# Kernel tuning notes

Hardware: AMD Instinct MI355X
Metric: run time of the kernel (lower is better)

The kernel has to match this reference:

```python
import jax, jax.numpy as jnp
import numpy as np

B = 4096       # batch
N_IN = 784     # input neurons
BANKS = 64     # banks per layer
L = 16         # layers of banks (layer 0 = input banks)
FAN = 8        # fan-out per source bank into next layer
D = 10         # n_neurons_per_hidd_bank
N_CONN = (L - 1) * BANKS * FAN  # total bank connections (7680)


def setup_inputs() -> dict:
    key = jax.random.key(0)
    ks = jax.random.split(key, 7)
    x = jax.random.normal(ks[0], (B, N_IN), jnp.float32)
    # input2hidden: Linear(N_IN, D, bias=True) for each input bank -> weight [D, N_IN]
    Wi = jax.random.normal(ks[1], (BANKS, D, N_IN), jnp.float32) / np.sqrt(N_IN).astype(np.float32)
    bi = jax.random.normal(ks[2], (BANKS, D), jnp.float32) * 0.1
    # per-edge gate: Linear(D, 1, bias=True); bias shifted so gates are a mix of open/closed
    Wg = jax.random.normal(ks[3], (L - 1, BANKS, FAN, D), jnp.float32) / np.sqrt(D).astype(np.float32)
    bg = jax.random.normal(ks[4], (L - 1, BANKS, FAN), jnp.float32) * 0.3 + 0.2
    # per-edge data: Linear(D, D, bias=False) -> weight [out=D, in=D]
    Wd = jax.random.normal(ks[5], (L - 1, BANKS, FAN, D, D), jnp.float32) / np.sqrt(D).astype(np.float32)
    # hidden2output: Linear(D, 1, bias=False) per output bank
    Wo = jax.random.normal(ks[6], (BANKS, D), jnp.float32) / np.sqrt(D).astype(np.float32)
    return {"x": x, "Wi": Wi, "bi": bi, "Wg": Wg, "bg": bg, "Wd": Wd, "Wo": Wo}


def reference(x, Wi, bi, Wg, bg, Wd, Wo):
    # forward_softgate with defaults: no batch norm, dropout p=0 (identity),
    # gates enabled (b_no_gates=False), positive gate loss, no gate_status.
    batch = x.shape[0]
    # static scatter targets: source bank s feeds banks (s+k)%BANKS of next layer
    s = np.arange(BANKS)[:, None]
    k = np.arange(FAN)[None, :]
    tgt = jnp.asarray(((s + k) % BANKS).reshape(-1))  # [BANKS*FAN]

    # input banks (layer 0); the target loop applies ReLU to every bank, incl. input banks
    acts = jax.nn.relu(jnp.einsum('bi,koi->bko', x, Wi) + bi)  # [B, BANKS, D]

    def layer(acts, w):
        wg, bgl, wd = w
        # gate: hardtanh(Linear(acts), 0, 1) per edge -> [B, BANKS, FAN]
        gate = jnp.clip(jnp.einsum('bsd,skd->bsk', acts, wg) + bgl, 0.0, 1.0)
        # data: Linear(D, D, bias=False); torch y = x @ W.T with W[out, in]
        data = jnp.einsum('bsd,sked->bske', acts, wd)  # [B, BANKS, FAN, D]
        contrib = (gate[..., None] * data).reshape(batch, BANKS * FAN, D)
        acc = jnp.zeros_like(acts).at[:, tgt].add(contrib)  # scatter-add into target banks
        new_acts = jax.nn.relu(acc)
        gate_sum = gate.sum(axis=(1, 2))                   # per-sample gate activity
        n_open = (gate > 0.0).sum().astype(jnp.float32)    # open-gate count
        return new_acts, (gate_sum, n_open)

    acts, (gate_sums, n_opens) = jax.lax.scan(layer, acts, (Wg, bg, Wd))
    total_gate_act = (gate_sums.sum(axis=0) / N_CONN)[:, None]          # [B, 1]
    prob_open_gate = n_opens.sum() / (N_CONN * batch)                   # scalar
    # output banks = last layer banks, Linear(D,1,bias=False) each, then ReLU
    output = jax.nn.relu(jnp.einsum('bkd,kd->bk', acts, Wo))            # [B, BANKS]
    return output, total_gate_act, prob_open_gate
```

## Files before the change

kernel.cpp:

```cpp
#include <hip/hip_runtime.h>
#include <type_traits>

#define NIN 784
#define BANKS 64
#define NLAYER 15
#define FAN 8
#define DD 10
#define NBF 640
#define NSW 4
#define NSB 8

#define BM 128
#define BN 64
#define BK 16

__global__ __launch_bounds__(256)
void input_gemm(const float* __restrict__ x, const float* __restrict__ Wi,
                const float* __restrict__ bi, float* __restrict__ acts)
{
    __shared__ float As[BK][BM + 4];
    __shared__ float Bs[BK][BN + 4];
    const int tid = threadIdx.x;
    const int tx = tid & 15, ty = tid >> 4;
    const int m0 = blockIdx.x * BM;
    const int n0 = blockIdx.y * BN;

    float acc[8][4];
#pragma unroll
    for (int i = 0; i < 8; ++i)
#pragma unroll
        for (int j = 0; j < 4; ++j) acc[i][j] = 0.f;

    for (int kb = 0; kb < NIN / BK; ++kb) {
#pragma unroll
        for (int i = 0; i < 2; ++i) {
            int flat = tid + 256 * i;
            int m = flat >> 2, kq = flat & 3;
            float4 v = *(const float4*)(x + (m0 + m) * NIN + kb * BK + kq * 4);
            As[kq*4+0][m] = v.x; As[kq*4+1][m] = v.y;
            As[kq*4+2][m] = v.z; As[kq*4+3][m] = v.w;
        }
        {
            int n = tid >> 2, kq = tid & 3;
            float4 v = *(const float4*)(Wi + (n0 + n) * NIN + kb * BK + kq * 4);
            Bs[kq*4+0][n] = v.x; Bs[kq*4+1][n] = v.y;
            Bs[kq*4+2][n] = v.z; Bs[kq*4+3][n] = v.w;
        }
        __syncthreads();
#pragma unroll
        for (int k = 0; k < BK; ++k) {
            float4 a0 = *(const float4*)(&As[k][ty*8]);
            float4 a1 = *(const float4*)(&As[k][ty*8+4]);
            float4 bb = *(const float4*)(&Bs[k][tx*4]);
            float av[8] = {a0.x,a0.y,a0.z,a0.w,a1.x,a1.y,a1.z,a1.w};
            float bv[4] = {bb.x,bb.y,bb.z,bb.w};
#pragma unroll
            for (int i = 0; i < 8; ++i)
#pragma unroll
                for (int j = 0; j < 4; ++j)
                    acc[i][j] = fmaf(av[i], bv[j], acc[i][j]);
        }
        __syncthreads();
    }
    float4 bv = *(const float4*)(bi + n0 + tx*4);
#pragma unroll
    for (int i = 0; i < 8; ++i) {
        int row = m0 + ty*8 + i;
        float4 o;
        o.x = fmaxf(acc[i][0] + bv.x, 0.f);
        o.y = fmaxf(acc[i][1] + bv.y, 0.f);
        o.z = fmaxf(acc[i][2] + bv.z, 0.f);
        o.w = fmaxf(acc[i][3] + bv.w, 0.f);
        *(float4*)(acts + row * NBF + n0 + tx*4) = o;
    }
}

__device__ __forceinline__ float f4c_rt(const float4& v, int c) {
    return c == 0 ? v.x : (c == 1 ? v.y : (c == 2 ? v.z : v.w));
}

typedef const __attribute__((address_space(1))) void gas_void;
typedef __attribute__((address_space(3))) void las_void;

__device__ __forceinline__ void gll16(const void* g, void* l) {
    __builtin_amdgcn_global_load_lds((gas_void*)g, (las_void*)l, 16, 0, 0);
}

#define NCH (NLAYER*FAN*28*64)
#define NBI (NLAYER*2*64)

__global__ __launch_bounds__(256)
void transpose_weights(const float* __restrict__ Wg, const float* __restrict__ bg,
                       const float* __restrict__ Wd,
                       float4* __restrict__ chunk_t, float4* __restrict__ bias_t)
{
    int tid = blockIdx.x * 256 + threadIdx.x;
    if (tid < NCH) {
        int b = tid & 63;
        int rk = tid >> 6;
        int r = rk % 28;
        int lk = rk / 28;
        int k = lk & 7;
        int l = lk >> 3;
        float4 v;
        if (r < 25) {
            v = ((const float4*)Wd)[(((size_t)(l*64+b)*8 + k)*25) + r];
        } else {
            int q = r - 25;
            size_t base = ((size_t)(l*64+b)*8 + k)*10 + 4*q;
            float t[4];
#pragma unroll
            for (int c = 0; c < 4; ++c)
                t[c] = (4*q + c < 10) ? Wg[base + c] : 0.f;
            v = make_float4(t[0], t[1], t[2], t[3]);
        }
        chunk_t[tid] = v;
    } else if (tid < NCH + NBI) {
        int t2 = tid - NCH;
        int b = t2 & 63;
        int q = (t2 >> 6) & 1;
        int l = t2 >> 7;
        bias_t[t2] = ((const float4*)bg)[(size_t)(l*64+b)*2 + q];
    }
}

template<bool CT>
__global__ __launch_bounds__(256, 2)
void routenet_v5(const float* __restrict__ acts0,
                 const float* __restrict__ x, const float* __restrict__ Wi,
                 const float* __restrict__ bi,
                 const float* __restrict__ Wg, const float* __restrict__ bg,
                 const float* __restrict__ Wd, const float* __restrict__ Wo,
                 const float4* __restrict__ chunk_t, const float4* __restrict__ bias_t,
                 float* __restrict__ out, unsigned int* __restrict__ nopen_g)
{
    __shared__ float4 wdstage[2][28][64];
    __shared__ float4 biasbuf[2][2][64];
    __shared__ float  exch[2][NSW][5][64];

    const int tid  = threadIdx.x;
    const int lane = tid & 63;
    const int w    = tid >> 6;
    const int g    = w & 1;
    const int h    = w >> 1;
    const int b0   = blockIdx.x * NSB + g * NSW;

    float a[NSW][DD];

    if (acts0) {
#pragma unroll
        for (int s = 0; s < NSW; ++s) {
            const float2* p = (const float2*)(acts0 + (size_t)(b0 + s) * NBF + lane * DD);
#pragma unroll
            for (int d2 = 0; d2 < 5; ++d2) {
                float2 v = p[d2];
                a[s][d2*2]   = v.x;
                a[s][d2*2+1] = v.y;
            }
        }
    } else {
        for (int s = 0; s < NSW; ++s) {
            const float* xb = x + (size_t)(b0 + s) * NIN;
            for (int d = 0; d < DD; ++d) {
                int n = lane * DD + d;
                const float* wr = Wi + (size_t)n * NIN;
                float z = bi[n];
                for (int i = 0; i < NIN; ++i) z = fmaf(xb[i], wr[i], z);
                a[s][d] = fmaxf(z, 0.f);
            }
        }
    }

    float gsum[NSW];
#pragma unroll
    for (int s = 0; s < NSW; ++s) gsum[s] = 0.f;
    unsigned int nop = 0;

    auto stage_chunk = [&](int l, int k, int pdst) {
        if constexpr (CT) {
            const float4* base = chunk_t + (size_t)(l*8 + k) * 28 * 64;
#pragma unroll
            for (int j = 0; j < 7; ++j) {
                int r = w + 4 * j;
                gll16(base + r*64 + lane, &wdstage[pdst][r][0]);
            }
        } else {
            const float* wd_base = Wd + (size_t)l * (BANKS*FAN*DD*DD)
                                      + (size_t)lane * (FAN*DD*DD) + k * (DD*DD);
            const float* wg_base = Wg + (size_t)l * (BANKS*FAN*DD)
                                      + lane * (FAN*DD) + ((10*k) >> 2) * 4;
#pragma unroll
            for (int j = 0; j < 7; ++j) {
                int r = w + 4 * j;
                if (r < 25) gll16(wd_base + r * 4, &wdstage[pdst][r][0]);
                else        gll16(wg_base + (r - 25) * 4, &wdstage[pdst][r][0]);
            }
        }
    };
    auto stage_bias = [&](int l) {
        int q = w & 1;
        if constexpr (CT) {
            gll16(bias_t + (size_t)(l*2 + q)*64 + lane, &biasbuf[l & 1][q][0]);
        } else {
            gll16(bg + (size_t)l * (BANKS*FAN) + lane * FAN + q * 4,
                  &biasbuf[l & 1][q][0]);
        }
    };

    stage_chunk(0, 0, 0);
    stage_bias(0);
    asm volatile("s_waitcnt vmcnt(0)" ::: "memory");
    asm volatile("s_barrier" ::: "memory");

    for (int l = 0; l < NLAYER; ++l) {
        const int lp = l & 1;
        float acc[NSW][5];
#pragma unroll
        for (int s = 0; s < NSW; ++s)
#pragma unroll
            for (int el = 0; el < 5; ++el) acc[s][el] = 0.f;

        auto chunk_body = [&](auto Hc, int k, int p) {
            constexpr int H = Hc.value;
            float4 wgq[3];
#pragma unroll
            for (int q = 0; q < 3; ++q) wgq[q] = wdstage[p][25 + q][lane];
            const float bias = f4c_rt(biasbuf[lp][(k >> 2) & 1][lane], k & 3);
            float wgv[DD];
            if constexpr (CT) {
#pragma unroll
                for (int d = 0; d < DD; ++d) wgv[d] = f4c_rt(wgq[d >> 2], d & 3);
            } else {
                if ((k & 1) == 0) {
#pragma unroll
                    for (int d = 0; d < DD; ++d) wgv[d] = f4c_rt(wgq[d >> 2], d & 3);
                } else {
#pragma unroll
                    for (int d = 0; d < DD; ++d) wgv[d] = f4c_rt(wgq[(d+2) >> 2], (d+2) & 3);
                }
            }

            float gz[NSW];
#pragma unroll
            for (int s = 0; s < NSW; ++s) {
                float z = bias;
#pragma unroll
                for (int d = 0; d < DD; ++d) z = fmaf(a[s][d], wgv[d], z);
                float gate = fminf(fmaxf(z, 0.f), 1.f);
                if (H == 0) { gsum[s] += gate; nop += (z > 0.f) ? 1u : 0u; }
                gz[s] = gate;
            }

            float4 wv[13];
#pragma unroll
            for (int i = 0; i < 13; ++i) wv[i] = wdstage[p][12*H + i][lane];

            const int src = (lane - k) & 63;
#pragma unroll
            for (int el = 0; el < 5; ++el) {
#pragma unroll
                for (int s = 0; s < NSW; ++s) {
                    float dot = 0.f;
#pragma unroll
                    for (int d = 0; d < DD; ++d) {
                        const int idx = (5*H + el) * 10 + d - 48*H;
                        dot = fmaf(a[s][d], f4c_rt(wv[idx >> 2], idx & 3), dot);
                    }
                    acc[s][el] += __shfl(gz[s] * dot, src, 64);
                }
            }
        };

#pragma unroll
        for (int c = 0; c < 8; ++c) {
            const int p = c & 1;
            if (c < 7) {
                stage_chunk(l, c + 1, p ^ 1);
                asm volatile("s_waitcnt vmcnt(7)" ::: "memory");
            } else if (l + 1 < NLAYER) {
                stage_chunk(l + 1, 0, p ^ 1);
                stage_bias(l + 1);
                asm volatile("s_waitcnt vmcnt(8)" ::: "memory");
            } else {
                asm volatile("s_waitcnt vmcnt(0)" ::: "memory");
            }
            asm volatile("s_barrier" ::: "memory");

            if (h == 0) chunk_body(std::integral_constant<int,0>{}, c, p);
            else        chunk_body(std::integral_constant<int,1>{}, c, p);

            if (c < 7) {
                asm volatile("s_waitcnt lgkmcnt(0)" ::: "memory");
                asm volatile("s_barrier" ::: "memory");
            }
        }

        if (h == 0) {
#pragma unroll
            for (int s = 0; s < NSW; ++s)
#pragma unroll
                for (int el = 0; el < 5; ++el)
                    a[s][el] = fmaxf(acc[s][el], 0.f);
        } else {
#pragma unroll
            for (int s = 0; s < NSW; ++s)
#pragma unroll
                for (int el = 0; el < 5; ++el) {
                    a[s][5 + el] = fmaxf(acc[s][el], 0.f);
                    exch[g][s][el][lane] = a[s][5 + el];
                }
        }
        asm volatile("s_waitcnt lgkmcnt(0)" ::: "memory");
        asm volatile("s_barrier" ::: "memory");

        if (h == 0) {
#pragma unroll
            for (int s = 0; s < NSW; ++s)
#pragma unroll
                for (int el = 0; el < 5; ++el)
                    a[s][5 + el] = exch[g][s][el][lane];
            if (l + 1 < NLAYER) {
#pragma unroll
                for (int s = 0; s < NSW; ++s)
#pragma unroll
                    for (int el = 0; el < 5; ++el)
                        exch[g][s][el][lane] = a[s][el];
            }
        }
        if (l + 1 < NLAYER) {
            asm volatile("s_waitcnt lgkmcnt(0)" ::: "memory");
            asm volatile("s_barrier" ::: "memory");
            if (h == 1) {
#pragma unroll
                for (int s = 0; s < NSW; ++s)
#pragma unroll
                    for (int el = 0; el < 5; ++el)
                        a[s][el] = exch[g][s][el][lane];
            }
        }
    }

    if (h == 0) {
        float wo[DD];
        const float2* p = (const float2*)(Wo + lane * DD);
#pragma unroll
        for (int d2 = 0; d2 < 5; ++d2) {
            float2 v = p[d2];
            wo[d2*2] = v.x; wo[d2*2+1] = v.y;
        }
#pragma unroll
        for (int s = 0; s < NSW; ++s) {
            float v = 0.f;
#pragma unroll
            for (int d = 0; d < DD; ++d) v = fmaf(a[s][d], wo[d], v);
            out[(size_t)(b0 + s) * BANKS + lane] = fmaxf(v, 0.f);
        }

#pragma unroll
        for (int s = 0; s < NSW; ++s) {
            float v = gsum[s];
#pragma unroll
            for (int off = 32; off; off >>= 1) v += __shfl_xor(v, off, 64);
            if (lane == 0)
                out[(size_t)4096 * BANKS + b0 + s] = v * (1.0f / 7680.0f);
        }
        {
            unsigned int v = nop;
#pragma unroll
            for (int off = 32; off; off >>= 1) v += __shfl_xor(v, off, 64);
            if (lane == 0) atomicAdd(nopen_g, v);
        }
    }
}

__global__ void finalize_prob(const unsigned int* __restrict__ nopen,
                              float* __restrict__ out)
{
    out[4096*64 + 4096] = (float)(*nopen) / 31457280.0f;
}

extern "C" void kernel_launch(void* const* d_in, const int* in_sizes, int n_in,
                              void* d_out, int out_size, void* d_ws, size_t ws_size,
                              hipStream_t stream)
{
    const float* x  = (const float*)d_in[0];
    const float* Wi = (const float*)d_in[1];
    const float* bi = (const float*)d_in[2];
    const float* Wg = (const float*)d_in[3];
    const float* bg = (const float*)d_in[4];
    const float* Wd = (const float*)d_in[5];
    const float* Wo = (const float*)d_in[6];
    float* out = (float*)d_out;

    const size_t ACTS_BYTES  = (size_t)4096 * NBF * 4;
    const size_t CHUNK_BYTES = (size_t)NCH * 16;
    const size_t BIAS_BYTES  = (size_t)NBI * 16;
    const size_t FULL_BYTES  = ACTS_BYTES + CHUNK_BYTES + BIAS_BYTES + 64;

    bool full    = ws_size >= FULL_BYTES;
    bool actonly = !full && ws_size >= ACTS_BYTES + 64;

    float* acts0 = (full || actonly) ? (float*)d_ws : nullptr;
    float4* chunk_t = full ? (float4*)((char*)d_ws + ACTS_BYTES) : nullptr;
    float4* bias_t  = full ? (float4*)((char*)d_ws + ACTS_BYTES + CHUNK_BYTES) : nullptr;
    unsigned int* nopen = full
        ? (unsigned int*)((char*)d_ws + ACTS_BYTES + CHUNK_BYTES + BIAS_BYTES)
        : (actonly ? (unsigned int*)((char*)d_ws + ACTS_BYTES)
                   : (unsigned int*)d_ws);

    hipMemsetAsync(nopen, 0, 4, stream);

    if (acts0) {
        dim3 grid(4096 / BM, NBF / BN);
        input_gemm<<<grid, 256, 0, stream>>>(x, Wi, bi, acts0);
    }
    if (full) {
        transpose_weights<<<(NCH + NBI + 255) / 256, 256, 0, stream>>>(
            Wg, bg, Wd, chunk_t, bias_t);
        routenet_v5<true><<<4096 / NSB, 256, 0, stream>>>(
            acts0, x, Wi, bi, Wg, bg, Wd, Wo, chunk_t, bias_t, out, nopen);
    } else {
        routenet_v5<false><<<4096 / NSB, 256, 0, stream>>>(
            acts0, x, Wi, bi, Wg, bg, Wd, Wo, nullptr, nullptr, out, nopen);
    }
    finalize_prob<<<1, 1, 0, stream>>>(nopen, out);
}
```

Baseline: 302.1 us.

## Stream transposed weights directly into registers with double-buffered prefetch

The new main kernel drops the LDS staging of per-chunk gate and data weights. Each wave instead loads its half of the pre-transposed weights from global memory straight into two register buffers, prefetching the next chunk while computing the current one. This removes the LDS write/read traffic and the per-chunk barriers, but it raises register pressure and leaves global-load latency to the register double buffer and L2 hits. The fallback path is kept as a separate non-templated kernel.

Result: slower. 797.3 us (+164.0%).

```diff
diff --git a/kernel.cpp b/kernel.cpp
--- a/kernel.cpp
+++ b/kernel.cpp
@@ -124,15 +124,203 @@
     }
 }
 
-template<bool CT>
 __global__ __launch_bounds__(256, 2)
-void routenet_v5(const float* __restrict__ acts0,
+void routenet_v6(const float* __restrict__ acts0,
                  const float* __restrict__ x, const float* __restrict__ Wi,
                  const float* __restrict__ bi,
-                 const float* __restrict__ Wg, const float* __restrict__ bg,
-                 const float* __restrict__ Wd, const float* __restrict__ Wo,
                  const float4* __restrict__ chunk_t, const float4* __restrict__ bias_t,
+                 const float* __restrict__ Wo,
                  float* __restrict__ out, unsigned int* __restrict__ nopen_g)
+{
+    __shared__ float exch[2][NSW][5][64];
+
+    const int tid  = threadIdx.x;
+    const int lane = tid & 63;
+    const int w    = tid >> 6;
+    const int g    = w & 1;
+    const int h    = w >> 1;
+    const int b0   = blockIdx.x * NSB + g * NSW;
+
+    float a[NSW][DD];
+#pragma unroll
+    for (int s = 0; s < NSW; ++s) {
+        const float2* p = (const float2*)(acts0 + (size_t)(b0 + s) * NBF + lane * DD);
+#pragma unroll
+        for (int d2 = 0; d2 < 5; ++d2) {
+            float2 v = p[d2];
+            a[s][d2*2]   = v.x;
+            a[s][d2*2+1] = v.y;
+        }
+    }
+
+    float gsum[NSW];
+#pragma unroll
+    for (int s = 0; s < NSW; ++s) gsum[s] = 0.f;
+    unsigned int nop = 0;
+
+    auto run = [&](auto Hc) {
+        constexpr int H = Hc.value;
+
+        float4 wvA[13], wgA[3], wvB[13], wgB[3];
+
+        auto prefetch = [&](int l_, int k_, float4 (&wv)[13], float4 (&wg)[3]) {
+            const float4* p = chunk_t + (size_t)(l_ * 8 + k_) * (28 * 64) + lane;
+#pragma unroll
+            for (int r = 0; r < 13; ++r) wv[r] = p[(12*H + r) * 64];
+#pragma unroll
+            for (int q = 0; q < 3; ++q) wg[q] = p[(25 + q) * 64];
+        };
+
+        auto compute = [&](int k, const float4 (&wv)[13], const float4 (&wg)[3],
+                           float (&acc)[NSW][5], const float4& bq0, const float4& bq1) {
+            float wgv[DD];
+#pragma unroll
+            for (int d = 0; d < DD; ++d) wgv[d] = f4c_rt(wg[d >> 2], d & 3);
+            const float bias = f4c_rt((k >> 2) ? bq1 : bq0, k & 3);
+
+            float gz[NSW];
+#pragma unroll
+            for (int s = 0; s < NSW; ++s) {
+                float z = bias;
+#pragma unroll
+                for (int d = 0; d < DD; ++d) z = fmaf(a[s][d], wgv[d], z);
+                float gate = fminf(fmaxf(z, 0.f), 1.f);
+                if (H == 0) { gsum[s] += gate; nop += (z > 0.f) ? 1u : 0u; }
+                gz[s] = gate;
+            }
+
+            const int src = (lane - k) & 63;
+#pragma unroll
+            for (int el = 0; el < 5; ++el) {
+#pragma unroll
+                for (int s = 0; s < NSW; ++s) {
+                    float dot = 0.f;
+#pragma unroll
+                    for (int d = 0; d < DD; ++d) {
+                        const int idx = (5*H + el) * 10 + d - 48*H;
+                        dot = fmaf(a[s][d], f4c_rt(wv[idx >> 2], idx & 3), dot);
+                    }
+                    acc[s][el] += __shfl(gz[s] * dot, src, 64);
+                }
+            }
+        };
+
+        prefetch(0, 0, wvA, wgA);
+        float4 bq0 = bias_t[lane];
+        float4 bq1 = bias_t[64 + lane];
+
+        for (int l = 0; l < NLAYER; ++l) {
+            float acc[NSW][5];
+#pragma unroll
+            for (int s = 0; s < NSW; ++s)
+#pragma unroll
+                for (int el = 0; el < 5; ++el) acc[s][el] = 0.f;
+
+            float4 bn0 = bq0, bn1 = bq1;
+#pragma unroll
+            for (int cc = 0; cc < 4; ++cc) {
+                prefetch(l, 2*cc + 1, wvB, wgB);
+                compute(2*cc, wvA, wgA, acc, bq0, bq1);
+                if (cc < 3) {
+                    prefetch(l, 2*cc + 2, wvA, wgA);
+                } else if (l + 1 < NLAYER) {
+                    prefetch(l + 1, 0, wvA, wgA);
+                    bn0 = bias_t[(size_t)((l+1) * 2)     * 64 + lane];
+                    bn1 = bias_t[(size_t)((l+1) * 2 + 1) * 64 + lane];
+                }
+                compute(2*cc + 1, wvB, wgB, acc, bq0, bq1);
+            }
+            bq0 = bn0; bq1 = bn1;
+
+            if (H == 0) {
+#pragma unroll
+                for (int s = 0; s < NSW; ++s)
+#pragma unroll
+                    for (int el = 0; el < 5; ++el)
+                        a[s][el] = fmaxf(acc[s][el], 0.f);
+            } else {
+#pragma unroll
+                for (int s = 0; s < NSW; ++s)
+#pragma unroll
+                    for (int el = 0; el < 5; ++el) {
+                        a[s][5 + el] = fmaxf(acc[s][el], 0.f);
+                        exch[g][s][el][lane] = a[s][5 + el];
+                    }
+            }
+            asm volatile("s_waitcnt lgkmcnt(0)" ::: "memory");
+            asm volatile("s_barrier" ::: "memory");
+
+            if (H == 0) {
+#pragma unroll
+                for (int s = 0; s < NSW; ++s)
+#pragma unroll
+                    for (int el = 0; el < 5; ++el)
+                        a[s][5 + el] = exch[g][s][el][lane];
+                if (l + 1 < NLAYER) {
+#pragma unroll
+                    for (int s = 0; s < NSW; ++s)
+#pragma unroll
+                        for (int el = 0; el < 5; ++el)
+                            exch[g][s][el][lane] = a[s][el];
+                }
+            }
+            if (l + 1 < NLAYER) {
+                asm volatile("s_waitcnt lgkmcnt(0)" ::: "memory");
+                asm volatile("s_barrier" ::: "memory");
+                if (H == 1) {
+#pragma unroll
+                    for (int s = 0; s < NSW; ++s)
+#pragma unroll
+                        for (int el = 0; el < 5; ++el)
+                            a[s][el] = exch[g][s][el][lane];
+                }
+            }
+        }
+    };
+
+    if (h == 0) run(std::integral_constant<int,0>{});
+    else        run(std::integral_constant<int,1>{});
+
+    if (h == 0) {
+        float wo[DD];
+        const float2* p = (const float2*)(Wo + lane * DD);
+#pragma unroll
+        for (int d2 = 0; d2 < 5; ++d2) {
+            float2 v = p[d2];
+            wo[d2*2] = v.x; wo[d2*2+1] = v.y;
+        }
+#pragma unroll
+        for (int s = 0; s < NSW; ++s) {
+            float v = 0.f;
+#pragma unroll
+            for (int d = 0; d < DD; ++d) v = fmaf(a[s][d], wo[d], v);
+            out[(size_t)(b0 + s) * BANKS + lane] = fmaxf(v, 0.f);
+        }
+
+#pragma unroll
+        for (int s = 0; s < NSW; ++s) {
+            float v = gsum[s];
+#pragma unroll
+            for (int off = 32; off; off >>= 1) v += __shfl_xor(v, off, 64);
+            if (lane == 0)
+                out[(size_t)4096 * BANKS + b0 + s] = v * (1.0f / 7680.0f);
+        }
+        {
+            unsigned int v = nop;
+#pragma unroll
+            for (int off = 32; off; off >>= 1) v += __shfl_xor(v, off, 64);
+            if (lane == 0) atomicAdd(nopen_g, v);
+        }
+    }
+}
+
+__global__ __launch_bounds__(256, 2)
+void routenet_v5f(const float* __restrict__ acts0,
+                  const float* __restrict__ x, const float* __restrict__ Wi,
+                  const float* __restrict__ bi,
+                  const float* __restrict__ Wg, const float* __restrict__ bg,
+                  const float* __restrict__ Wd, const float* __restrict__ Wo,
+                  float* __restrict__ out, unsigned int* __restrict__ nopen_g)
 {
     __shared__ float4 wdstage[2][28][64];
     __shared__ float4 biasbuf[2][2][64];
@@ -177,34 +365,21 @@
     unsigned int nop = 0;
 
     auto stage_chunk = [&](int l, int k, int pdst) {
-        if constexpr (CT) {
-            const float4* base = chunk_t + (size_t)(l*8 + k) * 28 * 64;
-#pragma unroll
-            for (int j = 0; j < 7; ++j) {
-                int r = w + 4 * j;
-                gll16(base + r*64 + lane, &wdstage[pdst][r][0]);
-            }
-        } else {
-            const float* wd_base = Wd + (size_t)l * (BANKS*FAN*DD*DD)
-                                      + (size_t)lane * (FAN*DD*DD) + k * (DD*DD);
-            const float* wg_base = Wg + (size_t)l * (BANKS*FAN*DD)
-                                      + lane * (FAN*DD) + ((10*k) >> 2) * 4;
-#pragma unroll
-            for (int j = 0; j < 7; ++j) {
-                int r = w + 4 * j;
-                if (r < 25) gll16(wd_base + r * 4, &wdstage[pdst][r][0]);
-                else        gll16(wg_base + (r - 25) * 4, &wdstage[pdst][r][0]);
-            }
+        const float* wd_base = Wd + (size_t)l * (BANKS*FAN*DD*DD)
+                                  + (size_t)lane * (FAN*DD*DD) + k * (DD*DD);
+        const float* wg_base = Wg + (size_t)l * (BANKS*FAN*DD)
+                                  + lane * (FAN*DD) + ((10*k) >> 2) * 4;
+#pragma unroll
+        for (int j = 0; j < 7; ++j) {
+            int r = w + 4 * j;
+            if (r < 25) gll16(wd_base + r * 4, &wdstage[pdst][r][0]);
+            else        gll16(wg_base + (r - 25) * 4, &wdstage[pdst][r][0]);
         }
     };
     auto stage_bias = [&](int l) {
         int q = w & 1;
-        if constexpr (CT) {
-            gll16(bias_t + (size_t)(l*2 + q)*64 + lane, &biasbuf[l & 1][q][0]);
-        } else {
-            gll16(bg + (size_t)l * (BANKS*FAN) + lane * FAN + q * 4,
-                  &biasbuf[l & 1][q][0]);
-        }
+        gll16(bg + (size_t)l * (BANKS*FAN) + lane * FAN + q * 4,
+              &biasbuf[l & 1][q][0]);
     };
 
     stage_chunk(0, 0, 0);
@@ -227,17 +402,12 @@
             for (int q = 0; q < 3; ++q) wgq[q] = wdstage[p][25 + q][lane];
             const float bias = f4c_rt(biasbuf[lp][(k >> 2) & 1][lane], k & 3);
             float wgv[DD];
-            if constexpr (CT) {
+            if ((k & 1) == 0) {
 #pragma unroll
                 for (int d = 0; d < DD; ++d) wgv[d] = f4c_rt(wgq[d >> 2], d & 3);
             } else {
-                if ((k & 1) == 0) {
-#pragma unroll
-                    for (int d = 0; d < DD; ++d) wgv[d] = f4c_rt(wgq[d >> 2], d & 3);
-                } else {
-#pragma unroll
-                    for (int d = 0; d < DD; ++d) wgv[d] = f4c_rt(wgq[(d+2) >> 2], (d+2) & 3);
-                }
+#pragma unroll
+                for (int d = 0; d < DD; ++d) wgv[d] = f4c_rt(wgq[(d+2) >> 2], (d+2) & 3);
             }
 
             float gz[NSW];
@@ -417,11 +587,11 @@
     if (full) {
         transpose_weights<<<(NCH + NBI + 255) / 256, 256, 0, stream>>>(
             Wg, bg, Wd, chunk_t, bias_t);
-        routenet_v5<true><<<4096 / NSB, 256, 0, stream>>>(
-            acts0, x, Wi, bi, Wg, bg, Wd, Wo, chunk_t, bias_t, out, nopen);
+        routenet_v6<<<4096 / NSB, 256, 0, stream>>>(
+            acts0, x, Wi, bi, chunk_t, bias_t, Wo, out, nopen);
     } else {
-        routenet_v5<false><<<4096 / NSB, 256, 0, stream>>>(
-            acts0, x, Wi, bi, Wg, bg, Wd, Wo, nullptr, nullptr, out, nopen);
+        routenet_v5f<<<4096 / NSB, 256, 0, stream>>>(
+            acts0, x, Wi, bi, Wg, bg, Wd, Wo, out, nopen);
     }
     finalize_prob<<<1, 1, 0, stream>>>(nopen, out);
 }
```
